# Kernel optimization log

Hardware: AMD Instinct MI355X
Metric: run time of the kernel (lower is better)

Reference implementation:

```python
import jax, jax.numpy as jnp
import numpy as np

E = 200_000       # num edges
A = 1_000_000     # num angle triplets
H = 128           # hidden_dim
BD = 8            # bilinear_dim
NR = 6            # num_radial_basis
NS = 7            # num_spherical_basis
MIN = 128         # message_in_dim
N_BEFORE = 1
N_AFTER = 2


def setup_inputs() -> dict:
    key = jax.random.key(0)
    ks = jax.random.split(key, 24)
    s = 0.05
    inp = {
        "distance_representation": jax.random.normal(ks[0], (E, NR), jnp.float32),
        "angle_representation": jax.random.normal(ks[1], (A, NS, NR), jnp.float32),
        "message": jax.random.normal(ks[2], (E, MIN), jnp.float32),
        "angle_index": jax.random.randint(ks[3], (2, A), 0, E),
        # parameters (stored as [in, out]; torch Linear applies x @ W.T)
        "W_dist": jax.random.normal(ks[4], (NR, H), jnp.float32) * s,
        "W_angle": jax.random.normal(ks[5], (NS * NR, BD), jnp.float32) * s,
        "W_src": jax.random.normal(ks[6], (MIN, H), jnp.float32) * s,
        "b_src": jnp.zeros((H,), jnp.float32),
        "W_tgt": jax.random.normal(ks[7], (MIN, H), jnp.float32) * s,
        "b_tgt": jnp.zeros((H,), jnp.float32),
        "W_bil": jax.random.normal(ks[8], (H, BD, H), jnp.float32) * (2.0 / H),
        "res_before_W": jax.random.normal(ks[9], (N_BEFORE, 2, H, H), jnp.float32) * s,
        "res_before_b": jnp.zeros((N_BEFORE, 2, H), jnp.float32),
        "W_skip": jax.random.normal(ks[10], (H, MIN), jnp.float32) * s,
        "b_skip": jnp.zeros((MIN,), jnp.float32),
        "res_after_W": jax.random.normal(ks[11], (N_AFTER, 2, MIN, MIN), jnp.float32) * s,
        "res_after_b": jnp.zeros((N_AFTER, 2, MIN), jnp.float32),
    }
    return inp


def _residual(x, Ws, bs, act):
    # x + act(L2(act(L1(x))))
    h = act(x @ Ws[0] + bs[0])
    h = act(h @ Ws[1] + bs[1])
    return x + h


def reference(distance_representation, angle_representation, message, angle_index,
              W_dist, W_angle, W_src, b_src, W_tgt, b_tgt, W_bil,
              res_before_W, res_before_b, W_skip, b_skip,
              res_after_W, res_after_b):
    act = jax.nn.silu
    num_edges = message.shape[0]
    num_angles = angle_index.shape[-1]

    d = distance_representation @ W_dist                       # [E, H]
    a = angle_representation.reshape(num_angles, -1) @ W_angle  # [A, BD]

    src_e, tgt_e = angle_index[0], angle_index[1]
    sm = message[src_e] @ W_src + b_src                        # [A, H] gather + linear
    sm = sm * d[tgt_e]                                         # [A, H]
    sm = jnp.einsum('ab,ah,ibh->ai', a, sm, W_bil)             # [A, H] bilinear

    agg = jax.ops.segment_sum(sm, tgt_e, num_segments=num_edges)  # [E, H] scatter-add

    x0 = message
    x = agg + (message @ W_tgt + b_tgt)
    for i in range(res_before_W.shape[0]):
        x = _residual(x, res_before_W[i], res_before_b[i], act)
    x = act(x @ W_skip + b_skip) + x0
    for i in range(res_after_W.shape[0]):
        x = _residual(x, res_after_W[i], res_after_b[i], act)
    return x
```

## Files before the change

### kernel.cpp

```cpp
#include <hip/hip_runtime.h>
#include <hip/hip_fp16.h>
#include <stdint.h>

#define E_N 200000
#define A_N 1000000

typedef short s16x8 __attribute__((ext_vector_type(8)));
typedef short s16x4 __attribute__((ext_vector_type(4)));
typedef float f32x4 __attribute__((ext_vector_type(4)));
typedef uint32_t u32x4 __attribute__((ext_vector_type(4)));
typedef uint32_t u32x2 __attribute__((ext_vector_type(2)));
typedef int i32x4 __attribute__((ext_vector_type(4)));
typedef _Float16 f16x8 __attribute__((ext_vector_type(8)));

__device__ __forceinline__ ushort f2bf(float f) {
  uint32_t x = __float_as_uint(f);
  uint32_t r = x + 0x7FFFu + ((x >> 16) & 1u);
  return (ushort)(r >> 16);
}

__device__ __forceinline__ ushort f2h(float f) {
  return __half_as_ushort(__float2half(f));
}

__device__ __forceinline__ uint32_t cvtpk(float lo, float hi) {
  uint32_t r;
  asm("v_cvt_pk_bf16_f32 %0, %1, %2" : "=v"(r) : "v"(lo), "v"(hi));
  return r;
}

__device__ __forceinline__ uint32_t pkmul(uint32_t a, uint32_t b) {
  uint32_t r;
  asm("v_pk_mul_f16 %0, %1, %2" : "=v"(r) : "v"(a), "v"(b));
  return r;
}

__device__ __forceinline__ float silu_f(float v) {
  return v * (1.0f / (1.0f + __expf(-v)));
}

__device__ __forceinline__ int swz(int row, int h) {
  return row * 128 + (h ^ ((row & 7) << 3));
}

__device__ __forceinline__ int sws(int r, int c) {
  return r * 64 + ((c & 63) ^ ((r & 7) << 3));
}

__device__ __forceinline__ void exchCtoB(ushort* scw, int r15, int hi,
                                         const f32x4* xv, s16x8* st) {
  u32x2 pk[8];
#pragma unroll
  for (int nt = 0; nt < 8; nt++) {
    pk[nt][0] = cvtpk(xv[nt][0], xv[nt][1]);
    pk[nt][1] = cvtpk(xv[nt][2], xv[nt][3]);
  }
#pragma unroll
  for (int nt = 0; nt < 4; nt++)
    *(u32x2*)&scw[sws(r15, nt * 16 + hi * 4)] = pk[nt];
#pragma unroll
  for (int k = 0; k < 2; k++)
    st[k] = *(const s16x8*)&scw[sws(r15, k * 32 + hi * 8)];
#pragma unroll
  for (int nt = 4; nt < 8; nt++)
    *(u32x2*)&scw[sws(r15, nt * 16 + hi * 4)] = pk[nt];
#pragma unroll
  for (int k = 2; k < 4; k++)
    st[k] = *(const s16x8*)&scw[sws(r15, k * 32 + hi * 8)];
}

__device__ __forceinline__ void exchBtoC(ushort* scw, int r15, int hi,
                                         const s16x8* stv, u32x2* mc) {
#pragma unroll
  for (int k = 0; k < 2; k++)
    *(s16x8*)&scw[sws(r15, k * 32 + hi * 8)] = stv[k];
#pragma unroll
  for (int nt = 0; nt < 4; nt++)
    mc[nt] = *(const u32x2*)&scw[sws(r15, nt * 16 + hi * 4)];
#pragma unroll
  for (int k = 2; k < 4; k++)
    *(s16x8*)&scw[sws(r15, k * 32 + hi * 8)] = stv[k];
#pragma unroll
  for (int nt = 4; nt < 8; nt++)
    mc[nt] = *(const u32x2*)&scw[sws(r15, nt * 16 + hi * 4)];
}

__global__ __launch_bounds__(256) void k_prep(
    const float* __restrict__ Wbil, const float* __restrict__ Wsrc,
    const float* __restrict__ Wtgt, const float* __restrict__ WresB,
    const float* __restrict__ Wskip, const float* __restrict__ WresA,
    const float* __restrict__ bsrc, const float* __restrict__ btgt,
    const float* __restrict__ bresB, const float* __restrict__ bskip,
    const float* __restrict__ bresA,
    ushort* __restrict__ wg_bil, ushort* __restrict__ wg_lin,
    float* __restrict__ bias_tab) {
  int tid = blockIdx.x * 256 + threadIdx.x;
  if (tid < 8 * 16384) {
    int b = tid >> 14, r = tid & 16383;
    int i = r >> 7, h = r & 127;
    wg_bil[b * 16384 + swz(i, h)] = f2h(Wbil[(i * 8 + b) * 128 + h]);
    return;
  }
  tid -= 8 * 16384;
  if (tid < 9 * 16384) {
    int s = tid >> 14, r = tid & 16383;
    int c = r >> 7, h = r & 127;
    const float* src;
    switch (s) {
      case 0: src = Wsrc; break;
      case 1: src = Wtgt; break;
      case 2: src = WresB; break;
      case 3: src = WresB + 16384; break;
      case 4: src = Wskip; break;
      case 5: src = WresA; break;
      case 6: src = WresA + 16384; break;
      case 7: src = WresA + 32768; break;
      default: src = WresA + 49152; break;
    }
    wg_lin[s * 16384 + swz(c, h)] = f2bf(src[h * 128 + c]);
    return;
  }
  tid -= 9 * 16384;
  if (tid < 9 * 128) {
    int s = tid >> 7, c = tid & 127;
    const float* src;
    switch (s) {
      case 0: src = bsrc; break;
      case 1: src = btgt; break;
      case 2: src = bresB; break;
      case 3: src = bresB + 128; break;
      case 4: src = bskip; break;
      case 5: src = bresA; break;
      case 6: src = bresA + 128; break;
      case 7: src = bresA + 256; break;
      default: src = bresA + 384; break;
    }
    bias_tab[s * 128 + c] = src[c];
  }
}

__global__ __launch_bounds__(256) void k_hist(const int* __restrict__ aidx,
                                              int* __restrict__ cnt) {
  int i = blockIdx.x * 256 + threadIdx.x;
  if (i < A_N) atomicAdd(&cnt[aidx[A_N + i]], 1);
}

__global__ __launch_bounds__(256) void k_scan1(const int* __restrict__ cnt,
                                               int* __restrict__ excl,
                                               int* __restrict__ bsum) {
  __shared__ int s[256];
  int t = threadIdx.x;
  int base = blockIdx.x * 1024 + t * 4;
  int v[4];
#pragma unroll
  for (int j = 0; j < 4; j++) v[j] = (base + j < E_N) ? cnt[base + j] : 0;
  int sum = v[0] + v[1] + v[2] + v[3];
  s[t] = sum;
  __syncthreads();
#pragma unroll
  for (int d = 1; d < 256; d <<= 1) {
    int x = (t >= d) ? s[t - d] : 0;
    __syncthreads();
    s[t] += x;
    __syncthreads();
  }
  int run = s[t] - sum;
#pragma unroll
  for (int j = 0; j < 4; j++) {
    if (base + j < E_N) excl[base + j] = run;
    run += v[j];
  }
  if (t == 255) bsum[blockIdx.x] = s[255];
}

__global__ __launch_bounds__(256) void k_scan2(int* __restrict__ bsum, int nb) {
  __shared__ int s[256];
  int t = threadIdx.x;
  int orig = (t < nb) ? bsum[t] : 0;
  s[t] = orig;
  __syncthreads();
#pragma unroll
  for (int d = 1; d < 256; d <<= 1) {
    int x = (t >= d) ? s[t - d] : 0;
    __syncthreads();
    s[t] += x;
    __syncthreads();
  }
  if (t < nb) bsum[t] = s[t] - orig;
}

__global__ __launch_bounds__(256) void k_scan3(const int* __restrict__ excl,
                                               const int* __restrict__ bsum,
                                               int* __restrict__ cursor) {
  int t = threadIdx.x;
  int base = blockIdx.x * 1024 + t * 4;
  int add = bsum[blockIdx.x];
#pragma unroll
  for (int j = 0; j < 4; j++)
    if (base + j < E_N) cursor[base + j] = excl[base + j] + add;
}

__global__ __launch_bounds__(256) void k_scatter(const int* __restrict__ aidx,
                                                 int* __restrict__ cursor,
                                                 int* __restrict__ perm,
                                                 int* __restrict__ ste,
                                                 int* __restrict__ sse) {
  int i = blockIdx.x * 256 + threadIdx.x;
  if (i < A_N) {
    int te = aidx[A_N + i];
    int se = aidx[i];
    int pos = atomicAdd(&cursor[te], 1);
    perm[pos] = i;
    ste[pos] = te;
    sse[pos] = se;
  }
}

__global__ __launch_bounds__(256) void k_angle(const float* __restrict__ ang,
                                               const float* __restrict__ Wang,
                                               float* __restrict__ a_ws) {
  __shared__ float rows[128 * 42];
  __shared__ float wbuf[42 * 8];
  int t = threadIdx.x;
  int tile0 = blockIdx.x * 128;
  int nrows = A_N - tile0; if (nrows > 128) nrows = 128;
  if (nrows == 128) {
    const f32x4* src = (const f32x4*)(ang + (size_t)tile0 * 42);
    f32x4* dst = (f32x4*)rows;
    for (int k = t; k < 1344; k += 256) dst[k] = src[k];
  } else {
    int cnt = nrows * 42;
    for (int k = t; k < cnt; k += 256) rows[k] = ang[(size_t)tile0 * 42 + k];
  }
  for (int k = t; k < 336; k += 256) wbuf[k] = Wang[k];
  __syncthreads();
  int row = t >> 1, half = t & 1;
  if (row < nrows) {
    float a0 = 0.f, a1 = 0.f, a2 = 0.f, a3 = 0.f;
    const float* rp = &rows[row * 42];
    const float* wp = &wbuf[half * 4];
#pragma unroll
    for (int k = 0; k < 42; k++) {
      float v = rp[k];
      a0 += v * wp[k * 8 + 0]; a1 += v * wp[k * 8 + 1];
      a2 += v * wp[k * 8 + 2]; a3 += v * wp[k * 8 + 3];
    }
    f32x4 o; o.x = a0; o.y = a1; o.z = a2; o.w = a3;
    *(f32x4*)&a_ws[(tile0 + row) * 8 + half * 4] = o;
  }
}

__global__ __launch_bounds__(256) void k_asort(const int* __restrict__ perm,
                                               const float* __restrict__ a_ws,
                                               u32x4* __restrict__ a_srt) {
  int i = blockIdx.x * 256 + threadIdx.x;
  if (i >= A_N) return;
  int ga = perm[i];
  f32x4 a0 = *(const f32x4*)&a_ws[(size_t)ga * 8];
  f32x4 a1 = *(const f32x4*)&a_ws[(size_t)ga * 8 + 4];
  u32x4 o0, o1;
#pragma unroll
  for (int j = 0; j < 4; j++) {
    uint32_t h0 = f2h(a0[j]), h1 = f2h(a1[j]);
    o0[j] = (h0 << 16) | h0;
    o1[j] = (h1 << 16) | h1;
  }
  a_srt[(size_t)i * 2] = o0;
  a_srt[(size_t)i * 2 + 1] = o1;
}

__global__ __launch_bounds__(256) void k_dist(const float* __restrict__ dist,
                                              const float* __restrict__ Wd,
                                              ushort* __restrict__ dtab) {
  __shared__ float w[6 * 128];
  int t = threadIdx.x;
  for (int k = t; k < 768; k += 256) w[k] = Wd[k];
  __syncthreads();
  int gid = blockIdx.x * 256 + t;
  int e = gid >> 2, q = gid & 3;
  if (e >= E_N) return;
  float dv[6];
#pragma unroll
  for (int r = 0; r < 6; r++) dv[r] = dist[e * 6 + r];
#pragma unroll
  for (int j = 0; j < 32; j += 4) {
    int c = q * 32 + j;
    s16x4 o;
#pragma unroll
    for (int jj = 0; jj < 4; jj++) {
      float s = 0.f;
#pragma unroll
      for (int r = 0; r < 6; r++) s += dv[r] * w[r * 128 + c + jj];
      o[jj] = (short)f2h(s);
    }
    *(s16x4*)&dtab[e * 128 + c] = o;
  }
}

__global__ __launch_bounds__(512) void k_srcm(const float* __restrict__ msg,
                                              const ushort* __restrict__ wg_lin,
                                              const float* __restrict__ bias_tab,
                                              ushort* __restrict__ srcm) {
  __shared__ ushort xb[128 * 128];
  __shared__ ushort wb[16384];
  __shared__ float bias[128];
  int t = threadIdx.x;
  int tile0 = blockIdx.x * 128;
  const f32x4 Z4 = {0.f, 0.f, 0.f, 0.f};
  for (int off = t * 8; off < 16384; off += 4096)
    *(s16x8*)&wb[off] = *(const s16x8*)&wg_lin[off];
  if (t < 128) bias[t] = bias_tab[t];
  {
    int row = t >> 2, l = t & 3;
    int grow = tile0 + row;
#pragma unroll
    for (int j = 0; j < 8; j++) {
      int h = l * 32 + j * 4;
      s16x4 o; o[0] = 0; o[1] = 0; o[2] = 0; o[3] = 0;
      if (grow < E_N) {
        f32x4 v = *(const f32x4*)&msg[(size_t)grow * 128 + h];
        o[0] = (short)f2bf(v.x); o[1] = (short)f2bf(v.y);
        o[2] = (short)f2bf(v.z); o[3] = (short)f2bf(v.w);
      }
      *(s16x4*)&xb[swz(row, h)] = o;
    }
  }
  __syncthreads();
  int w = t >> 6, lane = t & 63;
  int rbase = w * 16;
  int arow = rbase + (lane & 15);
  int k0 = (lane >> 4) * 8;
  int r0 = (lane >> 4) * 4;
  f32x4 acc[8];
#pragma unroll
  for (int k = 0; k < 4; k++) {
    s16x8 af = *(const s16x8*)&xb[swz(arow, k * 32 + k0)];
#pragma unroll
    for (int nt = 0; nt < 8; nt++) {
      s16x8 bf = *(const s16x8*)&wb[swz(nt * 16 + (lane & 15), k * 32 + k0)];
      acc[nt] = __builtin_amdgcn_mfma_f32_16x16x32_bf16(af, bf, k == 0 ? Z4 : acc[nt], 0, 0, 0);
    }
  }
#pragma unroll
  for (int nt = 0; nt < 8; nt++) {
    int col = nt * 16 + (lane & 15);
    float bv = bias[col];
#pragma unroll
    for (int r = 0; r < 4; r++) {
      int grow = tile0 + rbase + r0 + r;
      if (grow < E_N) srcm[(size_t)grow * 128 + col] = f2h(acc[nt][r] + bv);
    }
  }
}

__global__ __launch_bounds__(256, 3) void k_bil(const int* __restrict__ sse,
                                                const ushort* __restrict__ srcm,
                                                const ushort* __restrict__ dtab,
                                                const u32x4* __restrict__ a_srt,
                                                const ushort* __restrict__ wg_bil,
                                                const int* __restrict__ ste,
                                                float* __restrict__ agg) {
  __shared__ ushort wb[16384];
  int t = threadIdx.x;
  int lane = t & 63, w = t >> 6;
  int tile0 = blockIdx.x * 128;
  int mb = w * 32;
  int r15 = lane & 15, hi = lane >> 4;
  int k0 = hi * 8;
  int r0 = hi * 4;
  const f32x4 Z4 = {0.f, 0.f, 0.f, 0.f};

  {
    const ushort* gs = wg_bil + w * 4096 + lane * 8;
    ushort* ls = &wb[w * 4096];
#pragma unroll
    for (int i = 0; i < 8; i++)
      __builtin_amdgcn_global_load_lds(
          (const __attribute__((address_space(1))) void*)(gs + i * 512),
          (__attribute__((address_space(3))) void*)(ls + i * 512), 16, 0, 0);
  }

  u32x4 smv[2][4];
  uint32_t avd[2][8];
  int teo[2][4];
#pragma unroll
  for (int mt = 0; mt < 2; mt++) {
    int grow = tile0 + mb + mt * 16 + r15;
    int ok = (grow < A_N);
    int se = ok ? sse[grow] : 0;
    int te = ok ? ste[grow] : 0;
    if (ok) {
      u32x4 o0 = a_srt[(size_t)grow * 2];
      u32x4 o1 = a_srt[(size_t)grow * 2 + 1];
#pragma unroll
      for (int j = 0; j < 4; j++) { avd[mt][j] = o0[j]; avd[mt][4 + j] = o1[j]; }
    } else {
#pragma unroll
      for (int j = 0; j < 8; j++) avd[mt][j] = 0u;
    }
#pragma unroll
    for (int k = 0; k < 4; k++) {
      u32x4 sv = *(const u32x4*)&srcm[(size_t)se * 128 + k * 32 + k0];
      u32x4 dv = *(const u32x4*)&dtab[(size_t)te * 128 + k * 32 + k0];
#pragma unroll
      for (int j = 0; j < 4; j++) smv[mt][k][j] = pkmul(sv[j], dv[j]);
    }
    int orow0 = tile0 + mb + mt * 16 + r0;
    if (orow0 + 3 < A_N) {
      i32x4 tq = *(const i32x4*)&ste[orow0];
#pragma unroll
      for (int r = 0; r < 4; r++) teo[mt][r] = tq[r];
    } else {
#pragma unroll
      for (int r = 0; r < 4; r++)
        teo[mt][r] = (orow0 + r < A_N) ? ste[orow0 + r] : 0;
    }
  }

  f32x4 OUT[2][8];
#pragma unroll
  for (int mt = 0; mt < 2; mt++)
#pragma unroll
    for (int nt = 0; nt < 8; nt++) OUT[mt][nt] = Z4;

  __syncthreads();

#pragma unroll
  for (int b = 0; b < 8; b++) {
    uint32_t a0b = avd[0][b], a1b = avd[1][b];
    __builtin_amdgcn_s_setprio(1);
#pragma unroll
    for (int k = 0; k < 4; k++) {
      u32x4 p0, p1;
#pragma unroll
      for (int j = 0; j < 4; j++) {
        p0[j] = pkmul(smv[0][k][j], a0b);
        p1[j] = pkmul(smv[1][k][j], a1b);
      }
      f16x8 af0 = __builtin_bit_cast(f16x8, p0);
      f16x8 af1 = __builtin_bit_cast(f16x8, p1);
#pragma unroll
      for (int nt = 0; nt < 8; nt++) {
        f16x8 bf = *(const f16x8*)&wb[swz(nt * 16 + r15, k * 32 + k0)];
        OUT[0][nt] = __builtin_amdgcn_mfma_f32_16x16x32_f16(af0, bf, OUT[0][nt], 0, 0, 0);
        OUT[1][nt] = __builtin_amdgcn_mfma_f32_16x16x32_f16(af1, bf, OUT[1][nt], 0, 0, 0);
      }
    }
    __builtin_amdgcn_s_setprio(0);
    if (b < 7) {
      __syncthreads();
      const ushort* gs = wg_bil + (b + 1) * 16384 + w * 4096 + lane * 8;
      ushort* ls = &wb[w * 4096];
#pragma unroll
      for (int i = 0; i < 8; i++)
        __builtin_amdgcn_global_load_lds(
            (const __attribute__((address_space(1))) void*)(gs + i * 512),
            (__attribute__((address_space(3))) void*)(ls + i * 512), 16, 0, 0);
      __syncthreads();
    }
  }

#pragma unroll
  for (int mt = 0; mt < 2; mt++) {
    float acc[8];
    int cte = teo[mt][0];
#pragma unroll
    for (int nt = 0; nt < 8; nt++) acc[nt] = OUT[mt][nt][0];
#pragma unroll
    for (int r = 1; r < 4; r++) {
      int nte = teo[mt][r];
      if (nte == cte) {
#pragma unroll
        for (int nt = 0; nt < 8; nt++) acc[nt] += OUT[mt][nt][r];
      } else {
        float* base = &agg[(size_t)cte * 128];
#pragma unroll
        for (int nt = 0; nt < 8; nt++)
          unsafeAtomicAdd(base + nt * 16 + r15, acc[nt]);
        cte = nte;
#pragma unroll
        for (int nt = 0; nt < 8; nt++) acc[nt] = OUT[mt][nt][r];
      }
    }
    float* base = &agg[(size_t)cte * 128];
#pragma unroll
    for (int nt = 0; nt < 8; nt++)
      unsafeAtomicAdd(base + nt * 16 + r15, acc[nt]);
  }
}

__global__ __launch_bounds__(512) void k_postA(const float* __restrict__ msg,
                                               const float* __restrict__ agg,
                                               const ushort* __restrict__ wg_lin,
                                               const float* __restrict__ bias_tab,
                                               ushort* __restrict__ xmid) {
  __shared__ ushort wb[4][16384];
  __shared__ ushort sc[8][1024];
  __shared__ float bias[4][128];
  int t = threadIdx.x;
  int lane = t & 63, w = t >> 6;
  int r15 = lane & 15, hi = lane >> 4;
  ushort* scw = &sc[w][0];
  const f32x4 Z4 = {0.f, 0.f, 0.f, 0.f};

#pragma unroll
  for (int s = 0; s < 4; s++) {
    const ushort* gs = wg_lin + (s + 1) * 16384 + t * 8;
    ushort* ls = &wb[s][t * 8];
#pragma unroll
    for (int i = 0; i < 4; i++)
      __builtin_amdgcn_global_load_lds(
          (const __attribute__((address_space(1))) void*)(gs + i * 4096),
          (__attribute__((address_space(3))) void*)(ls + i * 4096), 16, 0, 0);
  }
  if (t < 128) {
#pragma unroll
    for (int s = 0; s < 4; s++) bias[s][t] = bias_tab[(s + 1) * 128 + t];
  }
  __syncthreads();

#pragma unroll 1
  for (int tb = blockIdx.x; tb < 1563; tb += 256) {
    int r = tb * 128 + w * 16 + r15;
    bool ok = r < E_N;
    size_t gb = (size_t)r * 128;

    s16x8 st[4], mg[4];
#pragma unroll
    for (int k = 0; k < 4; k++) {
      f32x4 v0 = Z4, v1 = Z4;
      if (ok) {
        v0 = *(const f32x4*)&msg[gb + k * 32 + hi * 8];
        v1 = *(const f32x4*)&msg[gb + k * 32 + hi * 8 + 4];
      }
      u32x4 p;
      p[0] = cvtpk(v0.x, v0.y); p[1] = cvtpk(v0.z, v0.w);
      p[2] = cvtpk(v1.x, v1.y); p[3] = cvtpk(v1.z, v1.w);
      st[k] = __builtin_bit_cast(s16x8, p);
      mg[k] = st[k];
    }
    f32x4 ag[8];
#pragma unroll
    for (int nt = 0; nt < 8; nt++)
      ag[nt] = ok ? *(const f32x4*)&agg[gb + nt * 16 + hi * 4] : Z4;

    f32x4 xr[8], xv[8], C[8];

#pragma unroll
    for (int k = 0; k < 4; k++)
#pragma unroll
      for (int nt = 0; nt < 8; nt++) {
        s16x8 af = *(const s16x8*)&wb[0][swz(nt * 16 + r15, k * 32 + hi * 8)];
        C[nt] = __builtin_amdgcn_mfma_f32_16x16x32_bf16(af, st[k], k == 0 ? ag[nt] : C[nt], 0, 0, 0);
      }
#pragma unroll
    for (int nt = 0; nt < 8; nt++) {
      f32x4 bv = *(const f32x4*)&bias[0][nt * 16 + hi * 4];
#pragma unroll
      for (int q = 0; q < 4; q++) xv[nt][q] = C[nt][q] + bv[q];
      xr[nt] = xv[nt];
    }
    exchCtoB(scw, r15, hi, xv, st);

#pragma unroll
    for (int k = 0; k < 4; k++)
#pragma unroll
      for (int nt = 0; nt < 8; nt++) {
        s16x8 af = *(const s16x8*)&wb[1][swz(nt * 16 + r15, k * 32 + hi * 8)];
        C[nt] = __builtin_amdgcn_mfma_f32_16x16x32_bf16(af, st[k], k == 0 ? Z4 : C[nt], 0, 0, 0);
      }
#pragma unroll
    for (int nt = 0; nt < 8; nt++) {
      f32x4 bv = *(const f32x4*)&bias[1][nt * 16 + hi * 4];
#pragma unroll
      for (int q = 0; q < 4; q++) xv[nt][q] = silu_f(C[nt][q] + bv[q]);
    }
    exchCtoB(scw, r15, hi, xv, st);

#pragma unroll
    for (int k = 0; k < 4; k++)
#pragma unroll
      for (int nt = 0; nt < 8; nt++) {
        s16x8 af = *(const s16x8*)&wb[2][swz(nt * 16 + r15, k * 32 + hi * 8)];
        C[nt] = __builtin_amdgcn_mfma_f32_16x16x32_bf16(af, st[k], k == 0 ? Z4 : C[nt], 0, 0, 0);
      }
#pragma unroll
    for (int nt = 0; nt < 8; nt++) {
      f32x4 bv = *(const f32x4*)&bias[2][nt * 16 + hi * 4];
#pragma unroll
      for (int q = 0; q < 4; q++) xv[nt][q] = xr[nt][q] + silu_f(C[nt][q] + bv[q]);
    }
    exchCtoB(scw, r15, hi, xv, st);

#pragma unroll
    for (int k = 0; k < 4; k++)
#pragma unroll
      for (int nt = 0; nt < 8; nt++) {
        s16x8 af = *(const s16x8*)&wb[3][swz(nt * 16 + r15, k * 32 + hi * 8)];
        C[nt] = __builtin_amdgcn_mfma_f32_16x16x32_bf16(af, st[k], k == 0 ? Z4 : C[nt], 0, 0, 0);
      }
    u32x2 mc[8];
    exchBtoC(scw, r15, hi, mg, mc);
#pragma unroll
    for (int nt = 0; nt < 8; nt++) {
      f32x4 bv = *(const f32x4*)&bias[3][nt * 16 + hi * 4];
      f32x4 m0;
      m0[0] = __uint_as_float(mc[nt][0] << 16);
      m0[1] = __uint_as_float(mc[nt][0] & 0xffff0000u);
      m0[2] = __uint_as_float(mc[nt][1] << 16);
      m0[3] = __uint_as_float(mc[nt][1] & 0xffff0000u);
      u32x2 pk;
      float o0 = silu_f(C[nt][0] + bv[0]) + m0[0];
      float o1 = silu_f(C[nt][1] + bv[1]) + m0[1];
      float o2 = silu_f(C[nt][2] + bv[2]) + m0[2];
      float o3 = silu_f(C[nt][3] + bv[3]) + m0[3];
      pk[0] = cvtpk(o0, o1);
      pk[1] = cvtpk(o2, o3);
      if (ok) *(u32x2*)&xmid[gb + nt * 16 + hi * 4] = pk;
    }
  }
}

__global__ __launch_bounds__(512) void k_postB(const ushort* __restrict__ xmid,
                                               const ushort* __restrict__ wg_lin,
                                               const float* __restrict__ bias_tab,
                                               float* __restrict__ xout) {
  __shared__ ushort wb[4][16384];
  __shared__ ushort sc[8][1024];
  __shared__ float bias[4][128];
  int t = threadIdx.x;
  int lane = t & 63, w = t >> 6;
  int r15 = lane & 15, hi = lane >> 4;
  ushort* scw = &sc[w][0];
  const f32x4 Z4 = {0.f, 0.f, 0.f, 0.f};

#pragma unroll
  for (int s = 0; s < 4; s++) {
    const ushort* gs = wg_lin + (s + 5) * 16384 + t * 8;
    ushort* ls = &wb[s][t * 8];
#pragma unroll
    for (int i = 0; i < 4; i++)
      __builtin_amdgcn_global_load_lds(
          (const __attribute__((address_space(1))) void*)(gs + i * 4096),
          (__attribute__((address_space(3))) void*)(ls + i * 4096), 16, 0, 0);
  }
  if (t < 128) {
#pragma unroll
    for (int s = 0; s < 4; s++) bias[s][t] = bias_tab[(s + 5) * 128 + t];
  }
  __syncthreads();

#pragma unroll 1
  for (int tb = blockIdx.x; tb < 1563; tb += 256) {
    int r = tb * 128 + w * 16 + r15;
    bool ok = r < E_N;
    size_t gb = (size_t)r * 128;

    s16x8 st[4];
#pragma unroll
    for (int k = 0; k < 4; k++) {
      s16x8 z; u32x4 zz; zz[0] = 0; zz[1] = 0; zz[2] = 0; zz[3] = 0;
      z = __builtin_bit_cast(s16x8, zz);
      st[k] = ok ? *(const s16x8*)&xmid[gb + k * 32 + hi * 8] : z;
    }
    u32x2 mc[8];
    exchBtoC(scw, r15, hi, st, mc);
    f32x4 xr[8], xv[8], C[8];
#pragma unroll
    for (int nt = 0; nt < 8; nt++) {
      xr[nt][0] = __uint_as_float(mc[nt][0] << 16);
      xr[nt][1] = __uint_as_float(mc[nt][0] & 0xffff0000u);
      xr[nt][2] = __uint_as_float(mc[nt][1] << 16);
      xr[nt][3] = __uint_as_float(mc[nt][1] & 0xffff0000u);
    }

#pragma unroll
    for (int k = 0; k < 4; k++)
#pragma unroll
      for (int nt = 0; nt < 8; nt++) {
        s16x8 af = *(const s16x8*)&wb[0][swz(nt * 16 + r15, k * 32 + hi * 8)];
        C[nt] = __builtin_amdgcn_mfma_f32_16x16x32_bf16(af, st[k], k == 0 ? Z4 : C[nt], 0, 0, 0);
      }
#pragma unroll
    for (int nt = 0; nt < 8; nt++) {
      f32x4 bv = *(const f32x4*)&bias[0][nt * 16 + hi * 4];
#pragma unroll
      for (int q = 0; q < 4; q++) xv[nt][q] = silu_f(C[nt][q] + bv[q]);
    }
    exchCtoB(scw, r15, hi, xv, st);

#pragma unroll
    for (int k = 0; k < 4; k++)
#pragma unroll
      for (int nt = 0; nt < 8; nt++) {
        s16x8 af = *(const s16x8*)&wb[1][swz(nt * 16 + r15, k * 32 + hi * 8)];
        C[nt] = __builtin_amdgcn_mfma_f32_16x16x32_bf16(af, st[k], k == 0 ? Z4 : C[nt], 0, 0, 0);
      }
#pragma unroll
    for (int nt = 0; nt < 8; nt++) {
      f32x4 bv = *(const f32x4*)&bias[1][nt * 16 + hi * 4];
#pragma unroll
      for (int q = 0; q < 4; q++) xv[nt][q] = xr[nt][q] + silu_f(C[nt][q] + bv[q]);
      xr[nt] = xv[nt];
    }
    exchCtoB(scw, r15, hi, xv, st);

#pragma unroll
    for (int k = 0; k < 4; k++)
#pragma unroll
      for (int nt = 0; nt < 8; nt++) {
        s16x8 af = *(const s16x8*)&wb[2][swz(nt * 16 + r15, k * 32 + hi * 8)];
        C[nt] = __builtin_amdgcn_mfma_f32_16x16x32_bf16(af, st[k], k == 0 ? Z4 : C[nt], 0, 0, 0);
      }
#pragma unroll
    for (int nt = 0; nt < 8; nt++) {
      f32x4 bv = *(const f32x4*)&bias[2][nt * 16 + hi * 4];
#pragma unroll
      for (int q = 0; q < 4; q++) xv[nt][q] = silu_f(C[nt][q] + bv[q]);
    }
    exchCtoB(scw, r15, hi, xv, st);

#pragma unroll
    for (int k = 0; k < 4; k++)
#pragma unroll
      for (int nt = 0; nt < 8; nt++) {
        s16x8 af = *(const s16x8*)&wb[3][swz(nt * 16 + r15, k * 32 + hi * 8)];
        C[nt] = __builtin_amdgcn_mfma_f32_16x16x32_bf16(af, st[k], k == 0 ? Z4 : C[nt], 0, 0, 0);
      }
#pragma unroll
    for (int nt = 0; nt < 8; nt++) {
      f32x4 bv = *(const f32x4*)&bias[3][nt * 16 + hi * 4];
      f32x4 o;
#pragma unroll
      for (int q = 0; q < 4; q++) o[q] = xr[nt][q] + silu_f(C[nt][q] + bv[q]);
      if (ok) *(f32x4*)&xout[gb + nt * 16 + hi * 4] = o;
    }
  }
}

extern "C" void kernel_launch(void* const* d_in, const int* in_sizes, int n_in,
                              void* d_out, int out_size, void* d_ws, size_t ws_size,
                              hipStream_t stream) {
  const float* dist  = (const float*)d_in[0];
  const float* ang   = (const float*)d_in[1];
  const float* msg   = (const float*)d_in[2];
  const int*   aidx  = (const int*)d_in[3];
  const float* Wd    = (const float*)d_in[4];
  const float* Wang  = (const float*)d_in[5];
  const float* Wsrc  = (const float*)d_in[6];
  const float* bsrc  = (const float*)d_in[7];
  const float* Wtgt  = (const float*)d_in[8];
  const float* btgt  = (const float*)d_in[9];
  const float* Wbil  = (const float*)d_in[10];
  const float* WresB = (const float*)d_in[11];
  const float* bresB = (const float*)d_in[12];
  const float* Wskip = (const float*)d_in[13];
  const float* bskip = (const float*)d_in[14];
  const float* WresA = (const float*)d_in[15];
  const float* bresA = (const float*)d_in[16];

  char* ws = (char*)d_ws;
  ushort* srcm_f16 = (ushort*)(ws + 0);
  ushort* dtab_f16 = (ushort*)(ws + 51200000LL);
  float*  a_ws     = (float*)(ws + 102400000LL);
  ushort* wg_bil   = (ushort*)(ws + 134400000LL);
  ushort* wg_lin   = (ushort*)(ws + 134662144LL);
  float*  bias_tab = (float*)(ws + 134957056LL);
  int*    cnt      = (int*)(ws + 134961664LL);
  int*    cursor   = (int*)(ws + 135761664LL);
  int*    excl     = (int*)(ws + 136561664LL);
  int*    bsum     = (int*)(ws + 137361664LL);
  int*    perm     = (int*)(ws + 137362688LL);
  int*    ste      = (int*)(ws + 141362688LL);
  ushort* xmid     = (ushort*)(ws + 145362688LL);
  int*    sse      = (int*)(ws + 196562688LL);
  u32x4*  a_srt    = (u32x4*)(ws + 200562688LL);
  float*  agg      = (float*)d_out;

  (void)in_sizes; (void)n_in; (void)out_size; (void)ws_size;

  const int NSCAN = (E_N + 1023) / 1024;

  hipMemsetAsync(d_out, 0, (size_t)E_N * 128 * 4, stream);
  hipMemsetAsync(cnt, 0, (size_t)E_N * 4, stream);
  k_prep<<<1093, 256, 0, stream>>>(Wbil, Wsrc, Wtgt, WresB, Wskip, WresA,
                                   bsrc, btgt, bresB, bskip, bresA,
                                   wg_bil, wg_lin, bias_tab);
  k_hist<<<3907, 256, 0, stream>>>(aidx, cnt);
  k_scan1<<<NSCAN, 256, 0, stream>>>(cnt, excl, bsum);
  k_scan2<<<1, 256, 0, stream>>>(bsum, NSCAN);
  k_scan3<<<NSCAN, 256, 0, stream>>>(excl, bsum, cursor);
  k_scatter<<<3907, 256, 0, stream>>>(aidx, cursor, perm, ste, sse);
  k_angle<<<7813, 256, 0, stream>>>(ang, Wang, a_ws);
  k_asort<<<3907, 256, 0, stream>>>(perm, a_ws, a_srt);
  k_dist<<<3125, 256, 0, stream>>>(dist, Wd, dtab_f16);
  k_srcm<<<1563, 512, 0, stream>>>(msg, wg_lin, bias_tab, srcm_f16);
  k_bil<<<7813, 256, 0, stream>>>(sse, srcm_f16, dtab_f16, a_srt, wg_bil,
                                  ste, agg);
  k_postA<<<256, 512, 0, stream>>>(msg, agg, wg_lin, bias_tab, xmid);
  k_postB<<<256, 512, 0, stream>>>(xmid, wg_lin, bias_tab, (float*)d_out);
}
```

Baseline: 800.1 us.

## Fuse angle sort into angle kernel and double-buffer bilinear weight loads

The scatter kernel now records each angle's sorted position, so the angle projection kernel writes its packed fp16 output straight to the sorted slot. This removes the separate k_asort pass and the intermediate fp32 angle buffer. The bilinear kernel's weight staging is split into 16 half-size chunks in a double-buffered LDS ring, and the next chunk is prefetched while the current one is consumed, which drops one barrier per step. Writes from k_angle become scattered, and whether the prefetch overlaps depends on when the async LDS loads complete relative to the single barrier.

```diff
diff --git a/kernel.cpp b/kernel.cpp
--- a/kernel.cpp
+++ b/kernel.cpp
@@ -202,7 +202,7 @@
 
 __global__ __launch_bounds__(256) void k_scatter(const int* __restrict__ aidx,
                                                  int* __restrict__ cursor,
-                                                 int* __restrict__ perm,
+                                                 int* __restrict__ apos,
                                                  int* __restrict__ ste,
                                                  int* __restrict__ sse) {
   int i = blockIdx.x * 256 + threadIdx.x;
@@ -210,7 +210,7 @@
     int te = aidx[A_N + i];
     int se = aidx[i];
     int pos = atomicAdd(&cursor[te], 1);
-    perm[pos] = i;
+    apos[i] = pos;
     ste[pos] = te;
     sse[pos] = se;
   }
@@ -218,7 +218,8 @@
 
 __global__ __launch_bounds__(256) void k_angle(const float* __restrict__ ang,
                                                const float* __restrict__ Wang,
-                                               float* __restrict__ a_ws) {
+                                               const int* __restrict__ apos,
+                                               u32x4* __restrict__ a_srt) {
   __shared__ float rows[128 * 42];
   __shared__ float wbuf[42 * 8];
   int t = threadIdx.x;
@@ -245,28 +246,13 @@
       a0 += v * wp[k * 8 + 0]; a1 += v * wp[k * 8 + 1];
       a2 += v * wp[k * 8 + 2]; a3 += v * wp[k * 8 + 3];
     }
-    f32x4 o; o.x = a0; o.y = a1; o.z = a2; o.w = a3;
-    *(f32x4*)&a_ws[(tile0 + row) * 8 + half * 4] = o;
-  }
-}
-
-__global__ __launch_bounds__(256) void k_asort(const int* __restrict__ perm,
-                                               const float* __restrict__ a_ws,
-                                               u32x4* __restrict__ a_srt) {
-  int i = blockIdx.x * 256 + threadIdx.x;
-  if (i >= A_N) return;
-  int ga = perm[i];
-  f32x4 a0 = *(const f32x4*)&a_ws[(size_t)ga * 8];
-  f32x4 a1 = *(const f32x4*)&a_ws[(size_t)ga * 8 + 4];
-  u32x4 o0, o1;
-#pragma unroll
-  for (int j = 0; j < 4; j++) {
-    uint32_t h0 = f2h(a0[j]), h1 = f2h(a1[j]);
-    o0[j] = (h0 << 16) | h0;
-    o1[j] = (h1 << 16) | h1;
-  }
-  a_srt[(size_t)i * 2] = o0;
-  a_srt[(size_t)i * 2 + 1] = o1;
+    int pos = apos[tile0 + row];
+    u32x4 o;
+    uint32_t h0 = f2h(a0), h1 = f2h(a1), h2 = f2h(a2), h3 = f2h(a3);
+    o[0] = (h0 << 16) | h0; o[1] = (h1 << 16) | h1;
+    o[2] = (h2 << 16) | h2; o[3] = (h3 << 16) | h3;
+    a_srt[(size_t)pos * 2 + half] = o;
+  }
 }
 
 __global__ __launch_bounds__(256) void k_dist(const float* __restrict__ dist,
@@ -360,7 +346,7 @@
                                                 const ushort* __restrict__ wg_bil,
                                                 const int* __restrict__ ste,
                                                 float* __restrict__ agg) {
-  __shared__ ushort wb[16384];
+  __shared__ ushort wb[2][8192];
   int t = threadIdx.x;
   int lane = t & 63, w = t >> 6;
   int tile0 = blockIdx.x * 128;
@@ -371,10 +357,10 @@
   const f32x4 Z4 = {0.f, 0.f, 0.f, 0.f};
 
   {
-    const ushort* gs = wg_bil + w * 4096 + lane * 8;
-    ushort* ls = &wb[w * 4096];
-#pragma unroll
-    for (int i = 0; i < 8; i++)
+    const ushort* gs = wg_bil + w * 2048 + lane * 8;
+    ushort* ls = &wb[0][w * 2048];
+#pragma unroll
+    for (int i = 0; i < 4; i++)
       __builtin_amdgcn_global_load_lds(
           (const __attribute__((address_space(1))) void*)(gs + i * 512),
           (__attribute__((address_space(3))) void*)(ls + i * 512), 16, 0, 0);
@@ -426,7 +412,19 @@
   __syncthreads();
 
 #pragma unroll
-  for (int b = 0; b < 8; b++) {
+  for (int s = 0; s < 16; s++) {
+    int b = s >> 1, half = s & 1;
+    int buf = s & 1;
+    if (s < 15) {
+      int ns = s + 1, nb = ns >> 1, nh = ns & 1;
+      const ushort* gs = wg_bil + nb * 16384 + nh * 8192 + w * 2048 + lane * 8;
+      ushort* ls = &wb[buf ^ 1][w * 2048];
+#pragma unroll
+      for (int i = 0; i < 4; i++)
+        __builtin_amdgcn_global_load_lds(
+            (const __attribute__((address_space(1))) void*)(gs + i * 512),
+            (__attribute__((address_space(3))) void*)(ls + i * 512), 16, 0, 0);
+    }
     uint32_t a0b = avd[0][b], a1b = avd[1][b];
     __builtin_amdgcn_s_setprio(1);
 #pragma unroll
@@ -440,24 +438,15 @@
       f16x8 af0 = __builtin_bit_cast(f16x8, p0);
       f16x8 af1 = __builtin_bit_cast(f16x8, p1);
 #pragma unroll
-      for (int nt = 0; nt < 8; nt++) {
-        f16x8 bf = *(const f16x8*)&wb[swz(nt * 16 + r15, k * 32 + k0)];
+      for (int ntl = 0; ntl < 4; ntl++) {
+        int nt = half * 4 + ntl;
+        f16x8 bf = *(const f16x8*)&wb[buf][swz(ntl * 16 + r15, k * 32 + k0)];
         OUT[0][nt] = __builtin_amdgcn_mfma_f32_16x16x32_f16(af0, bf, OUT[0][nt], 0, 0, 0);
         OUT[1][nt] = __builtin_amdgcn_mfma_f32_16x16x32_f16(af1, bf, OUT[1][nt], 0, 0, 0);
       }
     }
     __builtin_amdgcn_s_setprio(0);
-    if (b < 7) {
-      __syncthreads();
-      const ushort* gs = wg_bil + (b + 1) * 16384 + w * 4096 + lane * 8;
-      ushort* ls = &wb[w * 4096];
-#pragma unroll
-      for (int i = 0; i < 8; i++)
-        __builtin_amdgcn_global_load_lds(
-            (const __attribute__((address_space(1))) void*)(gs + i * 512),
-            (__attribute__((address_space(3))) void*)(ls + i * 512), 16, 0, 0);
-      __syncthreads();
-    }
+    __syncthreads();
   }
 
 #pragma unroll
@@ -762,7 +751,6 @@
   char* ws = (char*)d_ws;
   ushort* srcm_f16 = (ushort*)(ws + 0);
   ushort* dtab_f16 = (ushort*)(ws + 51200000LL);
-  float*  a_ws     = (float*)(ws + 102400000LL);
   ushort* wg_bil   = (ushort*)(ws + 134400000LL);
   ushort* wg_lin   = (ushort*)(ws + 134662144LL);
   float*  bias_tab = (float*)(ws + 134957056LL);
@@ -770,7 +758,7 @@
   int*    cursor   = (int*)(ws + 135761664LL);
   int*    excl     = (int*)(ws + 136561664LL);
   int*    bsum     = (int*)(ws + 137361664LL);
-  int*    perm     = (int*)(ws + 137362688LL);
+  int*    apos     = (int*)(ws + 137362688LL);
   int*    ste      = (int*)(ws + 141362688LL);
   ushort* xmid     = (ushort*)(ws + 145362688LL);
   int*    sse      = (int*)(ws + 196562688LL);
@@ -790,9 +778,8 @@
   k_scan1<<<NSCAN, 256, 0, stream>>>(cnt, excl, bsum);
   k_scan2<<<1, 256, 0, stream>>>(bsum, NSCAN);
   k_scan3<<<NSCAN, 256, 0, stream>>>(excl, bsum, cursor);
-  k_scatter<<<3907, 256, 0, stream>>>(aidx, cursor, perm, ste, sse);
-  k_angle<<<7813, 256, 0, stream>>>(ang, Wang, a_ws);
-  k_asort<<<3907, 256, 0, stream>>>(perm, a_ws, a_srt);
+  k_scatter<<<3907, 256, 0, stream>>>(aidx, cursor, apos, ste, sse);
+  k_angle<<<7813, 256, 0, stream>>>(ang, Wang, apos, a_srt);
   k_dist<<<3125, 256, 0, stream>>>(dist, Wd, dtab_f16);
   k_srcm<<<1563, 512, 0, stream>>>(msg, wg_lin, bias_tab, srcm_f16);
   k_bil<<<7813, 256, 0, stream>>>(sse, srcm_f16, dtab_f16, a_srt, wg_bil,
```

Measured after the change: 852.6 us. +6.6%, slower.
